# Kernel tuning notes

Hardware: AMD Instinct MI355X
Metric: run time of the kernel (lower is better)

Reference implementation:

```python
import jax, jax.numpy as jnp
import numpy as np


def trilinear_sample(vol, pos):
    """PyTorch-style grid_sample, mode='bilinear' (trilinear for 5D),
    padding_mode='zeros', align_corners=True.
    vol: [B, C, D, H, W]; pos: [B, N, 3] with (x, y, z) in [-1, 1]
    where x indexes W, y indexes H, z indexes D. Returns [B, C, N].
    """
    B, C, D, H, W = vol.shape
    # align_corners=True un-normalization
    ix = (pos[..., 0] + 1.0) * 0.5 * (W - 1)
    iy = (pos[..., 1] + 1.0) * 0.5 * (H - 1)
    iz = (pos[..., 2] + 1.0) * 0.5 * (D - 1)
    x0f, y0f, z0f = jnp.floor(ix), jnp.floor(iy), jnp.floor(iz)
    fx, fy, fz = ix - x0f, iy - y0f, iz - z0f
    x0, y0, z0 = x0f.astype(jnp.int32), y0f.astype(jnp.int32), z0f.astype(jnp.int32)
    x1, y1, z1 = x0 + 1, y0 + 1, z0 + 1

    volf = vol.reshape(B, C, D * H * W)

    def corner(xc, yc, zc, w):
        valid = ((xc >= 0) & (xc < W) & (yc >= 0) & (yc < H) & (zc >= 0) & (zc < D))
        idx = (jnp.clip(zc, 0, D - 1) * H + jnp.clip(yc, 0, H - 1)) * W + jnp.clip(xc, 0, W - 1)
        g = jnp.take_along_axis(volf, idx[:, None, :], axis=2)  # [B, C, N]
        return g * (w * valid)[:, None, :]

    out = (corner(x0, y0, z0, (1 - fx) * (1 - fy) * (1 - fz))
           + corner(x1, y0, z0, fx * (1 - fy) * (1 - fz))
           + corner(x0, y1, z0, (1 - fx) * fy * (1 - fz))
           + corner(x1, y1, z0, fx * fy * (1 - fz))
           + corner(x0, y0, z1, (1 - fx) * (1 - fy) * fz)
           + corner(x1, y0, z1, fx * (1 - fy) * fz)
           + corner(x0, y1, z1, (1 - fx) * fy * fz)
           + corner(x1, y1, z1, fx * fy * fz))
    return out  # [B, C, N]


def setup_inputs() -> dict:
    key = jax.random.key(0)
    k1, k2, k3, k4 = jax.random.split(key, 4)
    B, N, F_IN, C, D = 4, 40000, 128, 128, 16
    x = jax.random.normal(k1, (B, N, F_IN), dtype=jnp.float32)
    adj = jax.random.randint(k2, (2, 320000), 0, N, dtype=jnp.int64)
    conv_layer = jax.random.normal(k3, (B, C, D, D, D), dtype=jnp.float32)
    # ChebConv K=1 weight: out = x @ W; scaled so positions land mostly in [0, 1]
    W = jax.random.normal(k4, (F_IN, 3), dtype=jnp.float32) * 0.02 + 0.5 / F_IN
    return {"x": x, "adj": adj, "conv_layer": conv_layer, "W": W}


def reference(x, adj, conv_layer, W):
    # ChebConv with K=1, bias=False: T0(L) = I, so positions = x @ W. adj unused.
    positions = jnp.einsum('bnf,fo->bno', x, W)           # [B, N, 3]
    grid = 2.0 * positions - 1.0                           # normalize to [-1, 1]
    skip = trilinear_sample(conv_layer, grid)              # [B, C, N]
    skip = jnp.transpose(skip, (0, 2, 1))                  # [B, N, C]
    out = jnp.concatenate([x, skip, positions], axis=2)    # [B, N, F+C+3]
    return out, positions
```

## Files before the change

### kernel.cpp

```cpp
#include <hip/hip_runtime.h>

#define NPTS 40000
#define BDIM 4
#define FIN  128
#define CCH  128
#define DVOX 16
#define SVOL 4096
#define OROW 259

typedef float fx4 __attribute__((ext_vector_type(4)));

__global__ __launch_bounds__(256) void transpose_conv(const float* __restrict__ conv,
                                                      float* __restrict__ convt) {
    __shared__ float tile[128][65];
    const int b  = blockIdx.y;
    const int s0 = blockIdx.x * 64;
    const int t  = threadIdx.x;

    const float* src = conv + (size_t)b * 128 * SVOL;
    #pragma unroll
    for (int i = 0; i < 32; ++i) {
        int e  = t + 256 * i;
        int c  = e >> 6;
        int sl = e & 63;
        tile[c][sl] = src[(size_t)c * SVOL + s0 + sl];
    }
    __syncthreads();
    float* dst = convt + ((size_t)b * SVOL + s0) * 128;
    #pragma unroll
    for (int i = 0; i < 32; ++i) {
        int e  = t + 256 * i;
        int sl = e >> 7;
        int c  = e & 127;
        dst[(size_t)sl * 128 + c] = tile[c][sl];
    }
}

template <bool TR>
__global__ __launch_bounds__(256) void igsc_main(const float* __restrict__ x,
                                                 const float* __restrict__ vol,
                                                 const float* __restrict__ Wm,
                                                 float* __restrict__ out,
                                                 float* __restrict__ pos_out) {
    __shared__ float xs[64 * 132];
    __shared__ float Ws[FIN * 3];
    __shared__ float wgt[64][8];
    __shared__ int   idx8[64][8];
    __shared__ float ps[64][3];

    const int t  = threadIdx.x;
    const int b  = blockIdx.y;
    const int p0 = blockIdx.x * 64;

    const float* xsrc = x + ((size_t)b * NPTS + p0) * FIN;
    #pragma unroll
    for (int i = 0; i < 8; ++i) {
        int e  = t + 256 * i;
        int p  = e >> 5;
        int f4 = e & 31;
        fx4 v = __builtin_nontemporal_load(&((const fx4*)xsrc)[e]);
        ((fx4*)&xs[p * 132])[f4] = v;
    }
    if (t < 96) ((fx4*)Ws)[t] = ((const fx4*)Wm)[t];
    __syncthreads();

    {
        const int p = t >> 2, q = t & 3;
        const float* xr = &xs[p * 132];
        float a0 = 0.f, a1 = 0.f, a2 = 0.f;
        #pragma unroll
        for (int i = 0; i < 32; ++i) {
            int   f  = q + 4 * i;
            float xv = xr[f];
            a0 = fmaf(xv, Ws[f * 3 + 0], a0);
            a1 = fmaf(xv, Ws[f * 3 + 1], a1);
            a2 = fmaf(xv, Ws[f * 3 + 2], a2);
        }
        a0 += __shfl_xor(a0, 1); a0 += __shfl_xor(a0, 2);
        a1 += __shfl_xor(a1, 1); a1 += __shfl_xor(a1, 2);
        a2 += __shfl_xor(a2, 1); a2 += __shfl_xor(a2, 2);

        if (q == 0) {
            ps[p][0] = a0; ps[p][1] = a1; ps[p][2] = a2;
            float gx = 2.f * a0 - 1.f, gy = 2.f * a1 - 1.f, gz = 2.f * a2 - 1.f;
            float ix = (gx + 1.f) * 0.5f * 15.f;
            float iy = (gy + 1.f) * 0.5f * 15.f;
            float iz = (gz + 1.f) * 0.5f * 15.f;
            float x0f = floorf(ix), y0f = floorf(iy), z0f = floorf(iz);
            float fx = ix - x0f, fy = iy - y0f, fz = iz - z0f;
            int x0 = (int)x0f, y0 = (int)y0f, z0 = (int)z0f;
            #pragma unroll
            for (int k = 0; k < 8; ++k) {
                int dx = k & 1, dy = (k >> 1) & 1, dz = k >> 2;
                int xc = x0 + dx, yc = y0 + dy, zc = z0 + dz;
                bool valid = (xc >= 0) & (xc < DVOX) & (yc >= 0) & (yc < DVOX) &
                             (zc >= 0) & (zc < DVOX);
                int xcc = min(max(xc, 0), DVOX - 1);
                int ycc = min(max(yc, 0), DVOX - 1);
                int zcc = min(max(zc, 0), DVOX - 1);
                float wx = dx ? fx : 1.f - fx;
                float wy = dy ? fy : 1.f - fy;
                float wz = dz ? fz : 1.f - fz;
                wgt[p][k]  = valid ? wx * wy * wz : 0.f;
                idx8[p][k] = (zcc * DVOX + ycc) * DVOX + xcc;
            }
        }
    }
    __syncthreads();

    const int wave = t >> 6, lane = t & 63;
    const float* volb = vol + (size_t)b * SVOL * CCH;
    for (int pp = wave * 16; pp < wave * 16 + 16; ++pp) {
        float acc0 = 0.f, acc1 = 0.f;
        #pragma unroll
        for (int k = 0; k < 8; ++k) {
            float w = wgt[pp][k];
            if (w != 0.f) {
                int idx = idx8[pp][k];
                if (TR) {
                    const float2 v = ((const float2*)(volb + (size_t)idx * CCH))[lane];
                    acc0 = fmaf(w, v.x, acc0);
                    acc1 = fmaf(w, v.y, acc1);
                } else {
                    acc0 = fmaf(w, volb[(size_t)(2 * lane) * SVOL + idx], acc0);
                    acc1 = fmaf(w, volb[(size_t)(2 * lane + 1) * SVOL + idx], acc1);
                }
            }
        }
        size_t row  = (size_t)b * NPTS + p0 + pp;
        float* orow = out + row * OROW;
        __builtin_nontemporal_store(xs[pp * 132 + lane],      &orow[lane]);
        __builtin_nontemporal_store(xs[pp * 132 + 64 + lane], &orow[64 + lane]);
        __builtin_nontemporal_store(acc0, &orow[128 + 2 * lane]);
        __builtin_nontemporal_store(acc1, &orow[128 + 2 * lane + 1]);
        if (lane < 3) {
            float pv = ps[pp][lane];
            __builtin_nontemporal_store(pv, &orow[256 + lane]);
            __builtin_nontemporal_store(pv, &pos_out[row * 3 + lane]);
        }
    }
}

extern "C" void kernel_launch(void* const* d_in, const int* in_sizes, int n_in,
                              void* d_out, int out_size, void* d_ws, size_t ws_size,
                              hipStream_t stream) {
    const float* x    = (const float*)d_in[0];
    const float* conv = (const float*)d_in[2];
    const float* Wm   = (const float*)d_in[3];
    float* out     = (float*)d_out;
    float* pos_out = out + (size_t)BDIM * NPTS * OROW;

    const size_t need = (size_t)BDIM * SVOL * CCH * sizeof(float);
    if (ws_size >= need) {
        float* convt = (float*)d_ws;
        transpose_conv<<<dim3(SVOL / 64, BDIM), 256, 0, stream>>>(conv, convt);
        igsc_main<true><<<dim3(NPTS / 64, BDIM), 256, 0, stream>>>(x, convt, Wm, out, pos_out);
    } else {
        igsc_main<false><<<dim3(NPTS / 64, BDIM), 256, 0, stream>>>(x, conv, Wm, out, pos_out);
    }
}
```

Measured before the change: 264.2 us.

## Map batches to XCDs, drop x LDS staging, vectorize gather metadata

Launches a flat grid and remaps block IDs so each pair of XCDs handles one batch, keeping that batch's transposed volume in one XCD L2. Removes the shared-memory staging of x: each thread reads x straight from global for the projection, and x is re-read from global (likely an L2 hit) when the output row is written. Weights and indices are stored and loaded as vec4, and a 6-block occupancy hint is added. The trade is a second read of x in place of the LDS copy, in exchange for lower LDS use and higher occupancy.

```diff
diff --git a/kernel.cpp b/kernel.cpp
--- a/kernel.cpp
+++ b/kernel.cpp
@@ -9,6 +9,8 @@
 #define OROW 259
 
 typedef float fx4 __attribute__((ext_vector_type(4)));
+typedef float fx2 __attribute__((ext_vector_type(2)));
+typedef int   ix4 __attribute__((ext_vector_type(4)));
 
 __global__ __launch_bounds__(256) void transpose_conv(const float* __restrict__ conv,
                                                       float* __restrict__ convt) {
@@ -37,44 +39,49 @@
 }
 
 template <bool TR>
-__global__ __launch_bounds__(256) void igsc_main(const float* __restrict__ x,
-                                                 const float* __restrict__ vol,
-                                                 const float* __restrict__ Wm,
-                                                 float* __restrict__ out,
-                                                 float* __restrict__ pos_out) {
-    __shared__ float xs[64 * 132];
-    __shared__ float Ws[FIN * 3];
+__global__ __launch_bounds__(256, 6) void igsc_main(const float* __restrict__ x,
+                                                    const float* __restrict__ vol,
+                                                    const float* __restrict__ Wm,
+                                                    float* __restrict__ out,
+                                                    float* __restrict__ pos_out) {
+    __shared__ float Ws[4 * 100];
     __shared__ float wgt[64][8];
     __shared__ int   idx8[64][8];
     __shared__ float ps[64][3];
 
-    const int t  = threadIdx.x;
-    const int b  = blockIdx.y;
-    const int p0 = blockIdx.x * 64;
+    const int t    = threadIdx.x;
+    const int lid  = blockIdx.x;
+    const int xcd  = lid & 7;
+    const int b    = xcd >> 1;
+    const int slot = lid >> 3;
+    const int tile = slot + (xcd & 1) * 313;
+    if (tile >= 625) return;
+    const int p0 = tile * 64;
 
-    const float* xsrc = x + ((size_t)b * NPTS + p0) * FIN;
-    #pragma unroll
-    for (int i = 0; i < 8; ++i) {
-        int e  = t + 256 * i;
-        int p  = e >> 5;
-        int f4 = e & 31;
-        fx4 v = __builtin_nontemporal_load(&((const fx4*)xsrc)[e]);
-        ((fx4*)&xs[p * 132])[f4] = v;
+    for (int i = t; i < 384; i += 256) {
+        int f = i / 3, c = i - 3 * f;
+        Ws[(f >> 5) * 100 + (f & 31) * 3 + c] = Wm[i];
     }
-    if (t < 96) ((fx4*)Ws)[t] = ((const fx4*)Wm)[t];
     __syncthreads();
 
     {
         const int p = t >> 2, q = t & 3;
-        const float* xr = &xs[p * 132];
+        const float* xr = x + ((size_t)b * NPTS + p0 + p) * FIN + q * 32;
+        fx4 xv[8];
+        #pragma unroll
+        for (int j = 0; j < 8; ++j) xv[j] = ((const fx4*)xr)[j];
+        const float* wq = &Ws[q * 100];
         float a0 = 0.f, a1 = 0.f, a2 = 0.f;
         #pragma unroll
-        for (int i = 0; i < 32; ++i) {
-            int   f  = q + 4 * i;
-            float xv = xr[f];
-            a0 = fmaf(xv, Ws[f * 3 + 0], a0);
-            a1 = fmaf(xv, Ws[f * 3 + 1], a1);
-            a2 = fmaf(xv, Ws[f * 3 + 2], a2);
+        for (int j = 0; j < 8; ++j) {
+            #pragma unroll
+            for (int e = 0; e < 4; ++e) {
+                float xval = xv[j][e];
+                int   fl   = j * 4 + e;
+                a0 = fmaf(xval, wq[fl * 3 + 0], a0);
+                a1 = fmaf(xval, wq[fl * 3 + 1], a1);
+                a2 = fmaf(xval, wq[fl * 3 + 2], a2);
+            }
         }
         a0 += __shfl_xor(a0, 1); a0 += __shfl_xor(a0, 2);
         a1 += __shfl_xor(a1, 1); a1 += __shfl_xor(a1, 2);
@@ -89,6 +96,7 @@
             float x0f = floorf(ix), y0f = floorf(iy), z0f = floorf(iz);
             float fx = ix - x0f, fy = iy - y0f, fz = iz - z0f;
             int x0 = (int)x0f, y0 = (int)y0f, z0 = (int)z0f;
+            fx4 w0v, w1v; ix4 i0v, i1v;
             #pragma unroll
             for (int k = 0; k < 8; ++k) {
                 int dx = k & 1, dy = (k >> 1) & 1, dz = k >> 2;
@@ -101,36 +109,60 @@
                 float wx = dx ? fx : 1.f - fx;
                 float wy = dy ? fy : 1.f - fy;
                 float wz = dz ? fz : 1.f - fz;
-                wgt[p][k]  = valid ? wx * wy * wz : 0.f;
-                idx8[p][k] = (zcc * DVOX + ycc) * DVOX + xcc;
+                float wk = valid ? wx * wy * wz : 0.f;
+                int   ik = (zcc * DVOX + ycc) * DVOX + xcc;
+                if (k < 4) { w0v[k] = wk; i0v[k] = ik; }
+                else       { w1v[k - 4] = wk; i1v[k - 4] = ik; }
             }
+            *(fx4*)&wgt[p][0]  = w0v; *(fx4*)&wgt[p][4]  = w1v;
+            *(ix4*)&idx8[p][0] = i0v; *(ix4*)&idx8[p][4] = i1v;
         }
     }
     __syncthreads();
 
     const int wave = t >> 6, lane = t & 63;
     const float* volb = vol + (size_t)b * SVOL * CCH;
+    const float* xb   = x + ((size_t)b * NPTS + p0) * FIN;
+    #pragma unroll 4
     for (int pp = wave * 16; pp < wave * 16 + 16; ++pp) {
+        fx4 w0 = *(const fx4*)&wgt[pp][0];
+        fx4 w1 = *(const fx4*)&wgt[pp][4];
+        ix4 i0 = *(const ix4*)&idx8[pp][0];
+        ix4 i1 = *(const ix4*)&idx8[pp][4];
         float acc0 = 0.f, acc1 = 0.f;
         #pragma unroll
-        for (int k = 0; k < 8; ++k) {
-            float w = wgt[pp][k];
-            if (w != 0.f) {
-                int idx = idx8[pp][k];
+        for (int k = 0; k < 4; ++k) {
+            if (w0[k] != 0.f) {
+                int idx = i0[k];
                 if (TR) {
-                    const float2 v = ((const float2*)(volb + (size_t)idx * CCH))[lane];
-                    acc0 = fmaf(w, v.x, acc0);
-                    acc1 = fmaf(w, v.y, acc1);
+                    fx2 v = *(const fx2*)(volb + idx * CCH + 2 * lane);
+                    acc0 = fmaf(w0[k], v.x, acc0);
+                    acc1 = fmaf(w0[k], v.y, acc1);
                 } else {
-                    acc0 = fmaf(w, volb[(size_t)(2 * lane) * SVOL + idx], acc0);
-                    acc1 = fmaf(w, volb[(size_t)(2 * lane + 1) * SVOL + idx], acc1);
+                    acc0 = fmaf(w0[k], volb[(2 * lane) * SVOL + idx], acc0);
+                    acc1 = fmaf(w0[k], volb[(2 * lane + 1) * SVOL + idx], acc1);
+                }
+            }
+        }
+        #pragma unroll
+        for (int k = 0; k < 4; ++k) {
+            if (w1[k] != 0.f) {
+                int idx = i1[k];
+                if (TR) {
+                    fx2 v = *(const fx2*)(volb + idx * CCH + 2 * lane);
+                    acc0 = fmaf(w1[k], v.x, acc0);
+                    acc1 = fmaf(w1[k], v.y, acc1);
+                } else {
+                    acc0 = fmaf(w1[k], volb[(2 * lane) * SVOL + idx], acc0);
+                    acc1 = fmaf(w1[k], volb[(2 * lane + 1) * SVOL + idx], acc1);
                 }
             }
         }
         size_t row  = (size_t)b * NPTS + p0 + pp;
         float* orow = out + row * OROW;
-        __builtin_nontemporal_store(xs[pp * 132 + lane],      &orow[lane]);
-        __builtin_nontemporal_store(xs[pp * 132 + 64 + lane], &orow[64 + lane]);
+        fx2 xv2 = *(const fx2*)(xb + pp * FIN + 2 * lane);
+        __builtin_nontemporal_store(xv2.x, &orow[2 * lane]);
+        __builtin_nontemporal_store(xv2.y, &orow[2 * lane + 1]);
         __builtin_nontemporal_store(acc0, &orow[128 + 2 * lane]);
         __builtin_nontemporal_store(acc1, &orow[128 + 2 * lane + 1]);
         if (lane < 3) {
@@ -154,8 +186,8 @@
     if (ws_size >= need) {
         float* convt = (float*)d_ws;
         transpose_conv<<<dim3(SVOL / 64, BDIM), 256, 0, stream>>>(conv, convt);
-        igsc_main<true><<<dim3(NPTS / 64, BDIM), 256, 0, stream>>>(x, convt, Wm, out, pos_out);
+        igsc_main<true><<<dim3(313 * 8), 256, 0, stream>>>(x, convt, Wm, out, pos_out);
     } else {
-        igsc_main<false><<<dim3(NPTS / 64, BDIM), 256, 0, stream>>>(x, conv, Wm, out, pos_out);
+        igsc_main<false><<<dim3(313 * 8), 256, 0, stream>>>(x, conv, Wm, out, pos_out);
     }
 }
```

Result: slower. 283.9 us (+7.4%).
